# Kernel tuning notes

Measured on AMD Instinct MI355X. Metric: run time of the kernel, lower is better.

Reference implementation:

```python
import jax, jax.numpy as jnp
import numpy as np

B, S, D = 16, 577, 768   # batch, seq_len=(384//16)**2+1, hidden
H = 12                   # num heads
Dh = D // H              # head dim = 64
EPS = 1e-5


def setup_inputs() -> dict:
    key = jax.random.key(0)
    ks = jax.random.split(key, 12)
    sd = 0.02
    return {
        "x":    jax.random.normal(ks[0], (B, S, D), jnp.float32),
        "Wq":   jax.random.normal(ks[1], (D, 2 * D), jnp.float32) * sd,
        "bq":   jnp.zeros((2 * D,), jnp.float32),
        "Wk":   jax.random.normal(ks[2], (D, 2 * D), jnp.float32) * sd,
        "bk":   jnp.zeros((2 * D,), jnp.float32),
        "Wv":   jax.random.normal(ks[3], (D, D), jnp.float32) * sd,
        "bv":   jnp.zeros((D,), jnp.float32),
        "Wo":   jax.random.normal(ks[4], (D, D), jnp.float32) * sd,
        "bo":   jnp.zeros((D,), jnp.float32),
        "lam":  jnp.float32(0.5),
        "gn_w": jnp.ones((D,), jnp.float32),
        "gn_b": jnp.zeros((D,), jnp.float32),
    }


def _split_heads(t):
    # [B,S,D] -> [B,H,S,Dh]
    return t.reshape(B, S, H, Dh).transpose(0, 2, 1, 3)


def reference(x, Wq, bq, Wk, bk, Wv, bv, Wo, bo, lam, gn_w, gn_b):
    qc = x @ Wq + bq                      # [B,S,2D]
    kc = x @ Wk + bk
    v = _split_heads(x @ Wv + bv)         # [B,H,S,Dh]
    q1, q2 = _split_heads(qc[..., :D]), _split_heads(qc[..., D:])
    k1, k2 = _split_heads(kc[..., :D]), _split_heads(kc[..., D:])

    scale = 1.0 / np.sqrt(Dh).astype(np.float32)
    p1 = jax.nn.softmax(jnp.einsum('bhqd,bhkd->bhqk', q1, k1) * scale, axis=-1)
    p2 = jax.nn.softmax(jnp.einsum('bhqd,bhkd->bhqk', q2, k2) * scale, axis=-1)
    diff = p1 - lam * p2                  # [B,H,S,S] (dropout is identity at eval)
    ctx = jnp.einsum('bhqk,bhkd->bhqd', diff, v)   # [B,H,S,Dh]

    # GroupNorm path, faithfully reproducing the torch reshapes:
    # [B,H,S,Dh] -> permute -> [B,H,Dh,S] -> view [B, H*Dh, S]
    c = ctx.transpose(0, 1, 3, 2).reshape(B, H * Dh, S)
    g = c.reshape(B, H, Dh * S)
    mu = g.mean(axis=-1, keepdims=True)
    var = g.var(axis=-1, keepdims=True)
    g = (g - mu) * jax.lax.rsqrt(var + EPS)
    c = g.reshape(B, H * Dh, S) * gn_w[None, :, None] + gn_b[None, :, None]
    # torch then does permute(0,2,1).contiguous(); transpose(1,2).contiguous().view(B,S,D)
    # which nets out to reinterpreting the [B, H*Dh, S] buffer as [B, S, D]:
    context = c.reshape(B, S, D)

    out = context @ Wo + bo               # [B,S,D]
    return out
```

## Files before the change

### kernel.cpp

```cpp
#include <hip/hip_runtime.h>
#include <hip/hip_bf16.h>
#include <stdint.h>

typedef unsigned short u16;
typedef __attribute__((ext_vector_type(8))) short bf16x8;
typedef __attribute__((ext_vector_type(4))) float f32x4;

#define S_LEN 577
#define DMODEL 768
#define NHEAD 12
#define DH 64
#define BATCH 16
#define M_ROWS (BATCH * S_LEN)
#define M_PAD 9344
#define VT_STRIDE 640
#define CEXPF 0.18033688f

__device__ __forceinline__ u16 f2bu(float f) {
  uint32_t u = __float_as_uint(f);
  u += 0x7FFFu + ((u >> 16) & 1u);
  return (u16)(u >> 16);
}
__device__ __forceinline__ float bu2f(u16 b) {
  return __uint_as_float(((uint32_t)b) << 16);
}
__device__ __forceinline__ void gl2lds16(const u16* g, u16* l) {
  __builtin_amdgcn_global_load_lds(
      (const __attribute__((address_space(1))) unsigned int*)g,
      (__attribute__((address_space(3))) unsigned int*)l, 16, 0, 0);
}

__global__ __launch_bounds__(256) void prep_x(const float* __restrict__ x,
                                              u16* __restrict__ xb,
                                              float* __restrict__ stats) {
  if (blockIdx.x == 0 && threadIdx.x < 384) stats[threadIdx.x] = 0.f;
  int e = (blockIdx.x * 256 + threadIdx.x) * 8;
  u16 o[8];
  if (e < M_ROWS * DMODEL) {
    float4 f0 = *(const float4*)(x + e);
    float4 f1 = *(const float4*)(x + e + 4);
    o[0] = f2bu(f0.x); o[1] = f2bu(f0.y); o[2] = f2bu(f0.z); o[3] = f2bu(f0.w);
    o[4] = f2bu(f1.x); o[5] = f2bu(f1.y); o[6] = f2bu(f1.z); o[7] = f2bu(f1.w);
  } else {
#pragma unroll
    for (int i = 0; i < 8; ++i) o[i] = 0;
  }
  *(uint4*)(xb + e) = *(const uint4*)o;
}

__global__ __launch_bounds__(256) void prep_w(
    const float* __restrict__ Wq, const float* __restrict__ Wk,
    const float* __restrict__ Wv, const float* __restrict__ Wo,
    u16* __restrict__ wtqkv, u16* __restrict__ wot) {
  __shared__ u16 tile[32][33];
  int blk = blockIdx.x;
  const float* W; int N; u16* dst; int rowbase;
  if (blk < 1152)      { W = Wq; N = 1536; dst = wtqkv; rowbase = 0; }
  else if (blk < 2304) { W = Wk; N = 1536; dst = wtqkv; rowbase = 1536; blk -= 1152; }
  else if (blk < 2880) { W = Wv; N = 768;  dst = wtqkv; rowbase = 3072; blk -= 2304; }
  else                 { W = Wo; N = 768;  dst = wot;   rowbase = 0;    blk -= 2880; }
  const int ntiles = N >> 5;
  const int tk = blk / ntiles, tn = blk - tk * ntiles;
  const int c = threadIdx.x & 31, r0 = threadIdx.x >> 5;
#pragma unroll
  for (int i = 0; i < 4; ++i) {
    int r = i * 8 + r0;
    tile[r][c] = f2bu(W[(size_t)(tk * 32 + r) * N + tn * 32 + c]);
  }
  __syncthreads();
#pragma unroll
  for (int i = 0; i < 4; ++i) {
    int r = i * 8 + r0;
    dst[(size_t)(rowbase + tn * 32 + r) * 768 + tk * 32 + c] = tile[c][r];
  }
}

__global__ __launch_bounds__(256, 2) void gemm_bf16(
    const u16* __restrict__ A, const u16* __restrict__ Bt, int N, int mode,
    float* __restrict__ outF, const float* __restrict__ biasO,
    u16* __restrict__ q1p, u16* __restrict__ q2p,
    u16* __restrict__ k1p, u16* __restrict__ k2p, u16* __restrict__ vtp,
    const float* __restrict__ bq, const float* __restrict__ bk,
    const float* __restrict__ bvp) {
  __shared__ __align__(16) u16 smem[16384];
  const int t = threadIdx.x;
  const int lane = t & 63, wave = t >> 6;
  const int quad = lane >> 4, l16 = lane & 15;
  const int wm = wave & 1, wn = wave >> 1;

  const int NTg = gridDim.y;
  const int nwg = 73 * NTg;
  const int lin = blockIdx.y * 73 + blockIdx.x;
  const int xcd8 = lin & 7;
  const int idx8 = lin >> 3;
  const int qq = nwg >> 3, rr = nwg & 7;
  const int slot = (xcd8 < rr) ? xcd8 * (qq + 1) + idx8
                               : rr * (qq + 1) + (xcd8 - rr) * qq + idx8;
  const int C = (NTg >= 10) ? 5 : NTg;
  const int bpc = 73 * C;
  const int chunk = slot / bpc;
  const int rem = slot - chunk * bpc;
  const int mt = rem / C;
  const int nt = chunk * C + (rem - mt * C);
  const int m0 = mt * 128;
  const int n0 = nt * 128;

  f32x4 zero = {0.f, 0.f, 0.f, 0.f};
  f32x4 acc[4][4];
  for (int i = 0; i < 4; ++i) for (int j = 0; j < 4; ++j) acc[i][j] = zero;

  const int srow = wave * 32 + (lane >> 2);
  const int scol = ((lane & 3) ^ ((srow >> 1) & 3)) * 8;
  const u16* gA = A + (size_t)(m0 + srow) * 768 + scol;
  const u16* gB = Bt + (size_t)(n0 + srow) * 768 + scol;
  const int wofs = wave * 1024;
  const int xs = (quad ^ ((l16 >> 1) & 3)) * 8;

  {
    u16* sA = smem + wofs;
    u16* sB = smem + 4096 + wofs;
    gl2lds16(gA, sA);
    gl2lds16(gA + 16 * 768, sA + 512);
    gl2lds16(gB, sB);
    gl2lds16(gB + 16 * 768, sB + 512);
  }
  __syncthreads();

  int cur = 0;
  for (int k0 = 0; k0 < 768; k0 += 32) {
    if (k0 < 736) {
      u16* sA = smem + (cur ^ 1) * 8192 + wofs;
      u16* sB = smem + (cur ^ 1) * 8192 + 4096 + wofs;
      gl2lds16(gA + k0 + 32, sA);
      gl2lds16(gA + k0 + 32 + 16 * 768, sA + 512);
      gl2lds16(gB + k0 + 32, sB);
      gl2lds16(gB + k0 + 32 + 16 * 768, sB + 512);
    }
    const u16* cA = smem + cur * 8192;
    const u16* cB = smem + cur * 8192 + 4096;
    bf16x8 af[4], bfr[4];
#pragma unroll
    for (int i = 0; i < 4; ++i)
      af[i] = *(const bf16x8*)(cA + (wm * 64 + i * 16 + l16) * 32 + xs);
#pragma unroll
    for (int j = 0; j < 4; ++j)
      bfr[j] = *(const bf16x8*)(cB + (wn * 64 + j * 16 + l16) * 32 + xs);
#pragma unroll
    for (int i = 0; i < 4; ++i)
#pragma unroll
      for (int j = 0; j < 4; ++j)
        acc[i][j] = __builtin_amdgcn_mfma_f32_16x16x32_bf16(af[i], bfr[j], acc[i][j], 0, 0, 0);
    __syncthreads();
    cur ^= 1;
  }

  if (mode == 0) {
#pragma unroll
    for (int i = 0; i < 4; ++i) {
#pragma unroll
      for (int j = 0; j < 4; ++j) {
        int n = n0 + wn * 64 + j * 16 + l16;
#pragma unroll
        for (int r = 0; r < 4; ++r) {
          int m = m0 + wm * 64 + i * 16 + quad * 4 + r;
          if (m >= M_ROWS) continue;
          outF[(size_t)m * N + n] = acc[i][j][r] + biasO[n];
        }
      }
    }
    return;
  }

  u16* tile = smem;
  const bool isv = (n0 >= 3072);
  u16* dstqk = nullptr; const float* biasp = nullptr; int ch0 = 0;
  if (!isv) {
    if (n0 < 768)       { dstqk = q1p; biasp = bq + n0;          ch0 = n0; }
    else if (n0 < 1536) { dstqk = q2p; biasp = bq + n0;          ch0 = n0 - 768; }
    else if (n0 < 2304) { dstqk = k1p; biasp = bk + (n0 - 1536); ch0 = n0 - 1536; }
    else                { dstqk = k2p; biasp = bk + (n0 - 1536); ch0 = n0 - 2304; }
  }
  const float qscl = (n0 < 1536) ? CEXPF : 1.0f;
  const int ch0v = n0 - 3072;

#pragma unroll
  for (int hf = 0; hf < 2; ++hf) {
    __syncthreads();
    if (wn == hf) {
      if (!isv) {
        float bfv[4];
#pragma unroll
        for (int j = 0; j < 4; ++j) bfv[j] = biasp[hf * 64 + j * 16 + l16];
#pragma unroll
        for (int i = 0; i < 4; ++i)
#pragma unroll
          for (int j = 0; j < 4; ++j) {
            int col = j * 16 + l16;
#pragma unroll
            for (int r = 0; r < 4; ++r) {
              int m = wm * 64 + i * 16 + quad * 4 + r;
              int addr = m * 64 + (col & 15) + ((((col >> 4) ^ (m & 3)) & 3) << 4);
              tile[addr] = f2bu((acc[i][j][r] + bfv[j]) * qscl);
            }
          }
      } else {
        float bfv[4];
#pragma unroll
        for (int j = 0; j < 4; ++j) bfv[j] = bvp[ch0v + hf * 64 + j * 16 + l16];
#pragma unroll
        for (int i = 0; i < 4; ++i)
#pragma unroll
          for (int j = 0; j < 4; ++j) {
            int d = j * 16 + l16;
#pragma unroll
            for (int r = 0; r < 4; ++r) {
              int m = wm * 64 + i * 16 + quad * 4 + r;
              int addr = d * 128 + (m & 15) + ((((m >> 4) ^ (d & 7)) & 7) << 4);
              tile[addr] = f2bu(acc[i][j][r] + bfv[j]);
            }
          }
      }
    }
    __syncthreads();

    if (!isv) {
      const int line = t >> 3;
      const int col0 = (t & 7) * 8;
      const int head = (ch0 >> 6) + hf;
#pragma unroll
      for (int p = 0; p < 4; ++p) {
        int m = p * 32 + line;
        int mg = m0 + m;
        if (mg < M_ROWS) {
          int addr = m * 64 + (col0 & 15) + ((((col0 >> 4) ^ (m & 3)) & 3) << 4);
          uint4 v4 = *(const uint4*)(tile + addr);
          int b = mg / 577;
          int s = mg - b * 577;
          *(uint4*)(dstqk + (((size_t)(b * 12 + head) * 577 + s) * 64 + col0)) = v4;
        }
      }
    } else {
      const int line = t >> 4;
      const int col0 = (t & 15) * 8;
      const int hh = (ch0v >> 6) + hf;
#pragma unroll
      for (int p = 0; p < 4; ++p) {
        int d = p * 16 + line;
        int addr = d * 128 + (col0 & 15) + ((((col0 >> 4) ^ (d & 7)) & 7) << 4);
        uint4 v4 = *(const uint4*)(tile + addr);
        int sg0 = m0 + col0;
        int b0 = sg0 / 577, b7 = (sg0 + 7) / 577;
        if (sg0 + 7 < M_ROWS && b0 == b7) {
          *(uint4*)(vtp + (((size_t)(b0 * 12 + hh) * 64 + d) * VT_STRIDE + (sg0 - b0 * 577))) = v4;
        } else {
          const u16* ev = (const u16*)&v4;
          for (int e = 0; e < 8; ++e) {
            int sg = sg0 + e;
            if (sg >= M_ROWS) break;
            int bb = sg / 577;
            vtp[((size_t)(bb * 12 + hh) * 64 + d) * VT_STRIDE + (sg - bb * 577)] = ev[e];
          }
        }
      }
    }
  }
}

__global__ __launch_bounds__(256, 4) void attn(
    const u16* __restrict__ q1, const u16* __restrict__ q2,
    const u16* __restrict__ k1, const u16* __restrict__ k2,
    const u16* __restrict__ vt, u16* __restrict__ ctx_t,
    const float* __restrict__ lam_p, float* __restrict__ stats) {
  __shared__ u16 sk1[2][2048];
  __shared__ u16 sk2[2][2048];
  __shared__ u16 sv[2][2048];
  __shared__ u16 pls[4][2][16 * 40];

  const int tid = threadIdx.x;
  const int wave = tid >> 6;
  const int lane = tid & 63;
  const int quad = lane >> 4, l16 = lane & 15;

  const int bid = blockIdx.x;
  const int xcd = bid & 7;
  const int slot = bid >> 3;
  const int bhl = slot / 10;
  const int qgroup = slot - bhl * 10;
  const int bh = xcd * 24 + bhl;
  const int q0 = (qgroup * 4 + wave) * 16;
  const bool active = (q0 < S_LEN);

  const float lam = lam_p[0];
  const size_t qkbase = (size_t)bh * S_LEN * DH;
  const size_t vbase = (size_t)bh * 64 * VT_STRIDE;

  const int krow = tid >> 3;
  const int kelem = ((((tid & 7) << 4) ^ ((krow & 7) << 4)) >> 1);
  const u16* k1s = k1 + qkbase + (size_t)krow * 64 + kelem;
  const u16* k2s = k2 + qkbase + (size_t)krow * 64 + kelem;
  const int vrow = tid >> 2;
  const int vel = ((((tid & 3) << 4) ^ ((vrow & 3) << 4)) >> 1);
  const u16* vs = vt + vbase + (size_t)vrow * VT_STRIDE + vel;
  const int w512 = wave * 512;

  int qr = q0 + l16; if (qr > 576) qr = 576;
  bf16x8 q1f[2], q2f[2];
#pragma unroll
  for (int c = 0; c < 2; ++c) {
    q1f[c] = *(const bf16x8*)(q1 + qkbase + (size_t)qr * 64 + c * 32 + quad * 8);
    q2f[c] = *(const bf16x8*)(q2 + qkbase + (size_t)qr * 64 + c * 32 + quad * 8);
  }

  f32x4 zero = {0.f, 0.f, 0.f, 0.f};
  f32x4 O1[4], O2[4];
#pragma unroll
  for (int i = 0; i < 4; ++i) { O1[i] = zero; O2[i] = zero; }
  float l1p = 0.f, l2p = 0.f;

  u16* p1w = &pls[wave][0][0];
  u16* p2w = &pls[wave][1][0];

  const int xk = (l16 & 7) << 4;
  const int xv = (l16 & 3) << 4;

  gl2lds16(k1s, &sk1[0][0] + w512);
  gl2lds16(k2s, &sk2[0][0] + w512);
  gl2lds16(vs, &sv[0][0] + w512);
  __syncthreads();

  int cur = 0;
  for (int kb = 0; kb < 18; ++kb) {
    if (kb < 17) {
      gl2lds16(k1s + (kb + 1) * 2048, &sk1[cur ^ 1][0] + w512);
      gl2lds16(k2s + (kb + 1) * 2048, &sk2[cur ^ 1][0] + w512);
      gl2lds16(vs + (kb + 1) * 32, &sv[cur ^ 1][0] + w512);
    } else {
      gl2lds16(k1 + qkbase + 576 * 64 + kelem, &sk1[cur ^ 1][0] + w512);
      gl2lds16(k2 + qkbase + 576 * 64 + kelem, &sk2[cur ^ 1][0] + w512);
      gl2lds16(vs + 576, &sv[cur ^ 1][0] + w512);
    }

    if (active) {
      const char* bk1 = (const char*)&sk1[cur][0];
      const char* bk2 = (const char*)&sk2[cur][0];
      const char* bv = (const char*)&sv[cur][0];
      bf16x8 k1f[2][2], k2f[2][2], vf[4];
#pragma unroll
      for (int tt = 0; tt < 2; ++tt) {
        int rb = (tt * 16 + l16) * 128;
        k1f[tt][0] = *(const bf16x8*)(bk1 + rb + ((quad * 16) ^ xk));
        k1f[tt][1] = *(const bf16x8*)(bk1 + rb + ((64 + quad * 16) ^ xk));
        k2f[tt][0] = *(const bf16x8*)(bk2 + rb + ((quad * 16) ^ xk));
        k2f[tt][1] = *(const bf16x8*)(bk2 + rb + ((64 + quad * 16) ^ xk));
      }
#pragma unroll
      for (int tt = 0; tt < 4; ++tt)
        vf[tt] = *(const bf16x8*)(bv + (tt * 16 + l16) * 64 + ((quad * 16) ^ xv));

      f32x4 s1[2], s2[2];
      __builtin_amdgcn_s_setprio(1);
#pragma unroll
      for (int tt = 0; tt < 2; ++tt) {
        s1[tt] = __builtin_amdgcn_mfma_f32_16x16x32_bf16(k1f[tt][0], q1f[0], zero, 0, 0, 0);
        s1[tt] = __builtin_amdgcn_mfma_f32_16x16x32_bf16(k1f[tt][1], q1f[1], s1[tt], 0, 0, 0);
        s2[tt] = __builtin_amdgcn_mfma_f32_16x16x32_bf16(k2f[tt][0], q2f[0], zero, 0, 0, 0);
        s2[tt] = __builtin_amdgcn_mfma_f32_16x16x32_bf16(k2f[tt][1], q2f[1], s2[tt], 0, 0, 0);
      }
      __builtin_amdgcn_s_setprio(0);

#pragma unroll
      for (int tt = 0; tt < 2; ++tt) {
        float pa[4], pb[4];
#pragma unroll
        for (int i = 0; i < 4; ++i) {
          pa[i] = exp2f(s1[tt][i]); l1p += pa[i];
          pb[i] = exp2f(s2[tt][i]); l2p += pb[i];
        }
        uint2 wa, wb;
        wa.x = (__float_as_uint(pa[1]) & 0xffff0000u) | (__float_as_uint(pa[0]) >> 16);
        wa.y = (__float_as_uint(pa[3]) & 0xffff0000u) | (__float_as_uint(pa[2]) >> 16);
        wb.x = (__float_as_uint(pb[1]) & 0xffff0000u) | (__float_as_uint(pb[0]) >> 16);
        wb.y = (__float_as_uint(pb[3]) & 0xffff0000u) | (__float_as_uint(pb[2]) >> 16);
        *(uint2*)(p1w + l16 * 40 + tt * 16 + quad * 4) = wa;
        *(uint2*)(p2w + l16 * 40 + tt * 16 + quad * 4) = wb;
      }
      bf16x8 p1a = *(const bf16x8*)(p1w + l16 * 40 + quad * 8);
      bf16x8 p2a = *(const bf16x8*)(p2w + l16 * 40 + quad * 8);
      __builtin_amdgcn_s_setprio(1);
#pragma unroll
      for (int tt = 0; tt < 4; ++tt) {
        O1[tt] = __builtin_amdgcn_mfma_f32_16x16x32_bf16(p1a, vf[tt], O1[tt], 0, 0, 0);
        O2[tt] = __builtin_amdgcn_mfma_f32_16x16x32_bf16(p2a, vf[tt], O2[tt], 0, 0, 0);
      }
      __builtin_amdgcn_s_setprio(0);
    }
    __syncthreads();
    cur ^= 1;
  }

  if (active) {
    {
      const char* bk1 = (const char*)&sk1[cur][0];
      const char* bk2 = (const char*)&sk2[cur][0];
      const char* bv = (const char*)&sv[cur][0];
      int rb = l16 * 128;
      bf16x8 ka0 = *(const bf16x8*)(bk1 + rb + ((quad * 16) ^ xk));
      bf16x8 ka1 = *(const bf16x8*)(bk1 + rb + ((64 + quad * 16) ^ xk));
      bf16x8 kb0 = *(const bf16x8*)(bk2 + rb + ((quad * 16) ^ xk));
      bf16x8 kb1 = *(const bf16x8*)(bk2 + rb + ((64 + quad * 16) ^ xk));
      f32x4 s1t = __builtin_amdgcn_mfma_f32_16x16x32_bf16(ka0, q1f[0], zero, 0, 0, 0);
      s1t = __builtin_amdgcn_mfma_f32_16x16x32_bf16(ka1, q1f[1], s1t, 0, 0, 0);
      f32x4 s2t = __builtin_amdgcn_mfma_f32_16x16x32_bf16(kb0, q2f[0], zero, 0, 0, 0);
      s2t = __builtin_amdgcn_mfma_f32_16x16x32_bf16(kb1, q2f[1], s2t, 0, 0, 0);
      bf16x8 vf[4];
#pragma unroll
      for (int tt = 0; tt < 4; ++tt)
        vf[tt] = *(const bf16x8*)(bv + (tt * 16 + l16) * 64 + ((quad * 16) ^ xv));
      bool okp = (quad == 0);
      float pa[4], pb[4];
#pragma unroll
      for (int i = 0; i < 4; ++i) {
        pa[i] = (okp && i == 0) ? exp2f(s1t[i]) : 0.f;
        pb[i] = (okp && i == 0) ? exp2f(s2t[i]) : 0.f;
        l1p += pa[i]; l2p += pb[i];
      }
      uint2 wa, wb, wz;
      wa.x = (__float_as_uint(pa[1]) & 0xffff0000u) | (__float_as_uint(pa[0]) >> 16);
      wa.y = (__float_as_uint(pa[3]) & 0xffff0000u) | (__float_as_uint(pa[2]) >> 16);
      wb.x = (__float_as_uint(pb[1]) & 0xffff0000u) | (__float_as_uint(pb[0]) >> 16);
      wb.y = (__float_as_uint(pb[3]) & 0xffff0000u) | (__float_as_uint(pb[2]) >> 16);
      wz.x = 0; wz.y = 0;
      *(uint2*)(p1w + l16 * 40 + quad * 4) = wa;
      *(uint2*)(p1w + l16 * 40 + 16 + quad * 4) = wz;
      *(uint2*)(p2w + l16 * 40 + quad * 4) = wb;
      *(uint2*)(p2w + l16 * 40 + 16 + quad * 4) = wz;
      bf16x8 p1a = *(const bf16x8*)(p1w + l16 * 40 + quad * 8);
      bf16x8 p2a = *(const bf16x8*)(p2w + l16 * 40 + quad * 8);
#pragma unroll
      for (int tt = 0; tt < 4; ++tt) {
        O1[tt] = __builtin_amdgcn_mfma_f32_16x16x32_bf16(p1a, vf[tt], O1[tt], 0, 0, 0);
        O2[tt] = __builtin_amdgcn_mfma_f32_16x16x32_bf16(p2a, vf[tt], O2[tt], 0, 0, 0);
      }
    }

    l1p += __shfl_xor(l1p, 16); l1p += __shfl_xor(l1p, 32);
    l2p += __shfl_xor(l2p, 16); l2p += __shfl_xor(l2p, 32);
    float inv1 = 1.f / l1p, inv2 = 1.f / l2p;
    float a1[4], a2[4];
#pragma unroll
    for (int i = 0; i < 4; ++i) {
      a1[i] = __shfl(inv1, quad * 4 + i);
      a2[i] = __shfl(inv2, quad * 4 + i);
    }

    float ssum = 0.f, ssq = 0.f;
#pragma unroll
    for (int tt = 0; tt < 4; ++tt) {
      size_t cb = ((size_t)bh * 64 + tt * 16 + l16) * S_LEN;
#pragma unroll
      for (int i = 0; i < 4; ++i) {
        int s = q0 + quad * 4 + i;
        if (s < S_LEN) {
          float val = O1[tt][i] * a1[i] - lam * O2[tt][i] * a2[i];
          ctx_t[cb + s] = f2bu(val);
          ssum += val; ssq += val * val;
        }
      }
    }
#pragma unroll
    for (int d = 1; d < 64; d <<= 1) {
      ssum += __shfl_xor(ssum, d);
      ssq += __shfl_xor(ssq, d);
    }
    if (lane == 0) {
      atomicAdd(&stats[bh * 2], ssum);
      atomicAdd(&stats[bh * 2 + 1], ssq);
    }
  }
}

__global__ __launch_bounds__(256) void gnorm(
    const u16* __restrict__ ctx_t, u16* __restrict__ context,
    const float* __restrict__ gw, const float* __restrict__ gb,
    const float* __restrict__ stats) {
  const int bh = blockIdx.x;
  const int h = bh % 12;
  const int NEL = 64 * S_LEN;
  const int NV = NEL / 8;
  const u16* src = ctx_t + (size_t)bh * NEL;
  const float ts = stats[bh * 2];
  const float tq = stats[bh * 2 + 1];
  const float Ninv = 1.0f / (float)NEL;
  const float mu = ts * Ninv;
  const float var = tq * Ninv - mu * mu;
  const float rstd = rsqrtf(var + 1e-5f);
  __shared__ float wv[64], bv2[64];
  if (threadIdx.x < 64) {
    float w = gw[h * 64 + threadIdx.x] * rstd;
    wv[threadIdx.x] = w;
    bv2[threadIdx.x] = gb[h * 64 + threadIdx.x] - mu * w;
  }
  __syncthreads();
  u16* dst = context + (size_t)bh * NEL;
  for (int v = threadIdx.x; v < NV; v += 256) {
    uint4 raw = *(const uint4*)(src + v * 8);
    uint32_t w[4] = {raw.x, raw.y, raw.z, raw.w};
    int base = v * 8;
    int d0 = base / 577;
    int r0 = base - d0 * 577;
    u16 o[8];
#pragma unroll
    for (int j = 0; j < 4; ++j) {
#pragma unroll
      for (int e = 0; e < 2; ++e) {
        int ii = j * 2 + e;
        int dd = (r0 + ii >= 577) ? d0 + 1 : d0;
        float f = bu2f((u16)(e == 0 ? (w[j] & 0xffff) : (w[j] >> 16)));
        o[ii] = f2bu(f * wv[dd] + bv2[dd]);
      }
    }
    *(uint4*)(dst + base) = *(const uint4*)o;
  }
}

extern "C" void kernel_launch(void* const* d_in, const int* in_sizes, int n_in,
                              void* d_out, int out_size, void* d_ws, size_t ws_size,
                              hipStream_t stream) {
  const float* x   = (const float*)d_in[0];
  const float* Wq  = (const float*)d_in[1];
  const float* bq  = (const float*)d_in[2];
  const float* Wk  = (const float*)d_in[3];
  const float* bk  = (const float*)d_in[4];
  const float* Wv  = (const float*)d_in[5];
  const float* bv  = (const float*)d_in[6];
  const float* Wo  = (const float*)d_in[7];
  const float* bo  = (const float*)d_in[8];
  const float* lam = (const float*)d_in[9];
  const float* gw  = (const float*)d_in[10];
  const float* gb  = (const float*)d_in[11];
  float* out = (float*)d_out;

  char* p = (char*)d_ws;
  auto alloc = [&](size_t bytes) {
    char* r = p;
    p += (bytes + 255) & ~(size_t)255;
    return r;
  };
  u16* xb     = (u16*)alloc((size_t)M_PAD * 768 * 2);
  u16* wtqkv  = (u16*)alloc((size_t)3840 * 768 * 2);
  u16* wot    = (u16*)alloc((size_t)768 * 768 * 2);
  u16* q1b    = (u16*)alloc((size_t)192 * 577 * 64 * 2);
  u16* q2b    = (u16*)alloc((size_t)192 * 577 * 64 * 2);
  u16* k1b    = (u16*)alloc((size_t)192 * 577 * 64 * 2);
  u16* k2b    = (u16*)alloc((size_t)192 * 577 * 64 * 2);
  u16* vtb    = (u16*)alloc((size_t)192 * 64 * VT_STRIDE * 2);
  u16* ctxt   = (u16*)alloc((size_t)192 * 64 * S_LEN * 2);
  float* stats = (float*)alloc((size_t)192 * 2 * 4);
  u16* ctxbuf = xb;

  prep_x<<<(M_PAD * 768 / 8 + 255) / 256, 256, 0, stream>>>(x, xb, stats);
  prep_w<<<3456, 256, 0, stream>>>(Wq, Wk, Wv, Wo, wtqkv, wot);

  gemm_bf16<<<dim3(73, 30), 256, 0, stream>>>(xb, wtqkv, 3840, 1,
      nullptr, nullptr, q1b, q2b, k1b, k2b, vtb, bq, bk, bv);

  attn<<<dim3(1920), 256, 0, stream>>>(q1b, q2b, k1b, k2b, vtb, ctxt, lam, stats);

  gnorm<<<192, 256, 0, stream>>>(ctxt, ctxbuf, gw, gb, stats);

  gemm_bf16<<<dim3(73, 6), 256, 0, stream>>>(ctxbuf, wot, 768, 0,
      out, bo, nullptr, nullptr, nullptr, nullptr, nullptr, nullptr, nullptr, nullptr);
}
```

Measured before the change: 295.3 us.

## Triple-buffer GEMM LDS staging with prefetch distance two

Grows the GEMM shared-memory staging from two buffers to three and issues global-to-LDS loads two K-steps ahead. Explicit vmcnt waits let one stage's loads stay in flight across the barrier, replacing the full __syncthreads wait. This should hide more global memory latency behind the MFMA work. The cost is more LDS per block (48KB), which may cut occupancy, and the hand-written waitcnt counts must match the async load accounting exactly.

After: 295.5 us. No clear change (+0.1%).

```diff
diff --git a/kernel.cpp b/kernel.cpp
--- a/kernel.cpp
+++ b/kernel.cpp
@@ -82,7 +82,7 @@
     u16* __restrict__ k1p, u16* __restrict__ k2p, u16* __restrict__ vtp,
     const float* __restrict__ bq, const float* __restrict__ bk,
     const float* __restrict__ bvp) {
-  __shared__ __align__(16) u16 smem[16384];
+  __shared__ __align__(16) u16 smem[24576];
   const int t = threadIdx.x;
   const int lane = t & 63, wave = t >> 6;
   const int quad = lane >> 4, l16 = lane & 15;
@@ -117,24 +117,33 @@
   const int xs = (quad ^ ((l16 >> 1) & 3)) * 8;
 
   {
-    u16* sA = smem + wofs;
-    u16* sB = smem + 4096 + wofs;
-    gl2lds16(gA, sA);
-    gl2lds16(gA + 16 * 768, sA + 512);
-    gl2lds16(gB, sB);
-    gl2lds16(gB + 16 * 768, sB + 512);
-  }
-  __syncthreads();
+    u16* sA0 = smem + wofs;
+    u16* sB0 = smem + 4096 + wofs;
+    gl2lds16(gA, sA0);
+    gl2lds16(gA + 16 * 768, sA0 + 512);
+    gl2lds16(gB, sB0);
+    gl2lds16(gB + 16 * 768, sB0 + 512);
+    u16* sA1 = smem + 8192 + wofs;
+    u16* sB1 = smem + 8192 + 4096 + wofs;
+    gl2lds16(gA + 32, sA1);
+    gl2lds16(gA + 32 + 16 * 768, sA1 + 512);
+    gl2lds16(gB + 32, sB1);
+    gl2lds16(gB + 32 + 16 * 768, sB1 + 512);
+  }
+  asm volatile("s_waitcnt vmcnt(4)" ::: "memory");
+  __builtin_amdgcn_s_barrier();
+  __builtin_amdgcn_sched_barrier(0);
 
   int cur = 0;
   for (int k0 = 0; k0 < 768; k0 += 32) {
-    if (k0 < 736) {
-      u16* sA = smem + (cur ^ 1) * 8192 + wofs;
-      u16* sB = smem + (cur ^ 1) * 8192 + 4096 + wofs;
-      gl2lds16(gA + k0 + 32, sA);
-      gl2lds16(gA + k0 + 32 + 16 * 768, sA + 512);
-      gl2lds16(gB + k0 + 32, sB);
-      gl2lds16(gB + k0 + 32 + 16 * 768, sB + 512);
+    if (k0 < 704) {
+      int nx2 = cur + 2; if (nx2 >= 3) nx2 -= 3;
+      u16* sA = smem + nx2 * 8192 + wofs;
+      u16* sB = smem + nx2 * 8192 + 4096 + wofs;
+      gl2lds16(gA + k0 + 64, sA);
+      gl2lds16(gA + k0 + 64 + 16 * 768, sA + 512);
+      gl2lds16(gB + k0 + 64, sB);
+      gl2lds16(gB + k0 + 64 + 16 * 768, sB + 512);
     }
     const u16* cA = smem + cur * 8192;
     const u16* cB = smem + cur * 8192 + 4096;
@@ -150,8 +159,14 @@
 #pragma unroll
       for (int j = 0; j < 4; ++j)
         acc[i][j] = __builtin_amdgcn_mfma_f32_16x16x32_bf16(af[i], bfr[j], acc[i][j], 0, 0, 0);
-    __syncthreads();
-    cur ^= 1;
+    if (k0 < 704) {
+      asm volatile("s_waitcnt vmcnt(4)" ::: "memory");
+    } else {
+      asm volatile("s_waitcnt vmcnt(0)" ::: "memory");
+    }
+    __builtin_amdgcn_s_barrier();
+    __builtin_amdgcn_sched_barrier(0);
+    cur = (cur == 2) ? 0 : cur + 1;
   }
 
   if (mode == 0) {
```
